# Kernel tuning notes

Measured on AMD Instinct MI355X. Metric: run time of the kernel, lower is better.

The kernel has to match this reference:

```python
import jax, jax.numpy as jnp
import numpy as np

RADIUS = 0.1
K = 32
NUM_GROUPS = 8
EPS = 1e-5
B, N = 2, 4096
IN_DIM = 13
OUT_DIMS = (64, 64, 128)


def _safe_norm(x, axis=-1, keepdims=False):
    # 2-norm with zero (not NaN) gradient at 0; forward identical to jnp.linalg.norm
    sq = jnp.sum(x * x, axis=axis, keepdims=keepdims)
    nz = sq > 0
    return jnp.where(nz, jnp.sqrt(jnp.where(nz, sq, 1.0)), 0.0)


def _angle(v1, v2):
    y = _safe_norm(jnp.cross(v1, v2), axis=-1)
    x = jnp.sum(v1 * v2, axis=-1)
    deg = (y == 0) & (x == 0)  # degenerate pairs (e.g. self-neighbor): atan2(0,0)=0
    return jnp.where(deg, 0.0, jnp.arctan2(y, jnp.where(deg, 1.0, x)))


def _ball_group(xyz, radius, k):
    # xyz: (B,N,3) -> neighbor indices (B,N,K); pad out-of-radius slots with first valid idx
    b, n, _ = xyz.shape
    sq = jnp.sum((xyz[:, :, None, :] - xyz[:, None, :, :]) ** 2, axis=-1)  # (B,N,N)
    idx = jnp.broadcast_to(jnp.arange(n, dtype=jnp.int32), (b, n, n))
    idx = jnp.where(sq > radius * radius, n, idx)
    idx = jnp.sort(idx, axis=-1)[:, :, :k]  # (B,N,K)
    first = idx[:, :, :1]
    return jnp.where(idx == n, first, idx)


def _group_norm(x, gamma, beta):
    # x: (B,C,K,N), torch GroupNorm(8, C) semantics (biased var, eps=1e-5)
    b, c, k, n = x.shape
    xg = x.reshape(b, NUM_GROUPS, c // NUM_GROUPS, k, n)
    m = jnp.mean(xg, axis=(2, 3, 4), keepdims=True)
    v = jnp.var(xg, axis=(2, 3, 4), keepdims=True)
    xn = ((xg - m) * jax.lax.rsqrt(v + EPS)).reshape(b, c, k, n)
    return xn * gamma[None, :, None, None] + beta[None, :, None, None]


def _forward(feature, xyz, conv0_w, gn0_g, gn0_b, conv1_w, gn1_g, gn1_b,
             conv2_w, gn2_g, gn2_b, wa, wb, wc):
    b = xyz.shape[0]
    idx = _ball_group(xyz, RADIUS, K)                     # (B,N,K) int32
    bidx = jnp.arange(b)[:, None, None]
    grouped_xyz = xyz[bidx, idx]                          # (B,N,K,3)
    grouped_xyz1 = grouped_xyz - xyz[:, :, None, :]       # relative coords
    dists = _safe_norm(grouped_xyz1, axis=-1, keepdims=True)
    grouped_n = feature[bidx, idx]                        # grouped normals (B,N,K,3)
    new_points = jnp.concatenate([grouped_xyz1, dists, grouped_n], axis=-1)  # (B,N,K,7)

    nr = feature[:, :, None, :]                           # (B,N,1,3)
    ppf = jnp.stack([_angle(nr, grouped_xyz1),
                     _angle(grouped_n, grouped_xyz1),
                     _angle(nr, grouped_n)], axis=-1)     # (B,N,K,3)

    xyz6 = jnp.concatenate([jnp.broadcast_to(xyz[:, :, None, :], grouped_xyz.shape),
                            grouped_xyz], axis=-1)        # (B,N,K,6)
    fused = jnp.concatenate([wa * xyz6, wb * new_points[..., :4], wc * ppf], axis=-1)  # (B,N,K,13)

    x = jnp.transpose(fused, (0, 3, 2, 1))                # (B,13,K,N)
    layers = [(conv0_w, gn0_g, gn0_b), (conv1_w, gn1_g, gn1_b), (conv2_w, gn2_g, gn2_b)]
    for i, (w, g, bb) in enumerate(layers):
        x = jnp.einsum('oc,bckn->bokn', w, x)             # 1x1 conv, no bias
        x = _group_norm(x, g, bb)
        if i != len(layers) - 1:
            x = jax.nn.relu(x)
    out = jnp.max(jax.nn.relu(x), axis=2)                 # (B,128,N)
    x = jnp.max(x, axis=2)                                # (B,128,N)
    return (out, x)


def setup_inputs() -> dict:
    key = jax.random.key(0)
    ks = jax.random.split(key, 8)
    xyz = jax.random.uniform(ks[0], (B, N, 3), dtype=jnp.float32)
    feature = jax.random.normal(ks[1], (B, N, 3), dtype=jnp.float32)
    feature = feature / _safe_norm(feature, axis=-1, keepdims=True)  # unit normals
    inp = {'feature': feature, 'xyz': xyz}
    dims = [IN_DIM] + list(OUT_DIMS)
    for i in range(3):
        scale = 1.0 / np.sqrt(dims[i])
        inp[f'conv{i}_w'] = (jax.random.normal(ks[2 + i], (dims[i + 1], dims[i]), dtype=jnp.float32) * scale)
        inp[f'gn{i}_g'] = jnp.ones((dims[i + 1],), jnp.float32)
        inp[f'gn{i}_b'] = jnp.zeros((dims[i + 1],), jnp.float32)
    inp['wa'] = jnp.ones((1,), jnp.float32)
    inp['wb'] = jnp.ones((1,), jnp.float32)
    inp['wc'] = jnp.ones((1,), jnp.float32)
    return inp


def reference(feature, xyz, conv0_w, gn0_g, gn0_b, conv1_w, gn1_g, gn1_b,
              conv2_w, gn2_g, gn2_b, wa, wb, wc):
    return _forward(feature, xyz, conv0_w, gn0_g, gn0_b, conv1_w, gn1_g, gn1_b,
                    conv2_w, gn2_g, gn2_b, wa, wb, wc)
```

## Files before the change

kernel.cpp:

```cpp
#include <hip/hip_runtime.h>
#include <hip/hip_bf16.h>

#define DEVINL __device__ __forceinline__

typedef short short8 __attribute__((ext_vector_type(8)));
typedef float f32x4 __attribute__((ext_vector_type(4)));

namespace {
constexpr int NB = 2;
constexpr int NN = 4096;
constexpr int KK = 32;
constexpr int NP = NN * KK;
constexpr float R2 = 0.01f;
constexpr float GEPS = 1e-5f;
}

DEVINL ushort2 splitbf(float v) {
    unsigned int b = __float_as_uint(v);
    unsigned int hb = b & 0xffff0000u;
    float r = v - __uint_as_float(hb);
    unsigned int lb = __float_as_uint(r);
    ushort2 res;
    res.x = (unsigned short)(hb >> 16);
    res.y = (unsigned short)(lb >> 16);
    return res;
}

DEVINL float angle3(float ax, float ay, float az, float bx, float by, float bz) {
    float crx = ay * bz - az * by;
    float cry = az * bx - ax * bz;
    float crz = ax * by - ay * bx;
    float sq = crx * crx + cry * cry + crz * crz;
    float yv = sq > 0.f ? sqrtf(sq) : 0.f;
    float xv = ax * bx + ay * by + az * bz;
    if (yv == 0.f && xv == 0.f) return 0.f;
    return atan2f(yv, xv);
}

template <int NV>
DEVINL float blockReducePart(float* vals) {
    #pragma unroll
    for (int m = 1; m < 64; m <<= 1) {
        #pragma unroll
        for (int q = 0; q < NV; ++q) vals[q] += __shfl_xor(vals[q], m, 64);
    }
    __shared__ float red[4][NV];
    int lane = threadIdx.x & 63, w = threadIdx.x >> 6;
    if (lane == 0) {
        #pragma unroll
        for (int q = 0; q < NV; ++q) red[w][q] = vals[q];
    }
    __syncthreads();
    float v = 0.f;
    if ((int)threadIdx.x < NV)
        v = red[0][threadIdx.x] + red[1][threadIdx.x] +
            red[2][threadIdx.x] + red[3][threadIdx.x];
    return v;
}

__global__ __launch_bounds__(256) void k_red(const float* __restrict__ part,
                                             float* __restrict__ stats, int nblk) {
    int o = blockIdx.x;
    const float* p = part + (size_t)o * nblk;
    float s = 0.f;
    for (int i = threadIdx.x; i < nblk; i += 256) s += p[i];
    #pragma unroll
    for (int m = 1; m < 64; m <<= 1) s += __shfl_xor(s, m, 64);
    __shared__ float r[4];
    if ((threadIdx.x & 63) == 0) r[threadIdx.x >> 6] = s;
    __syncthreads();
    if (threadIdx.x == 0) stats[o] = r[0] + r[1] + r[2] + r[3];
}

__global__ void k_prep(const float* __restrict__ w0, const float* __restrict__ w1,
                       const float* __restrict__ w2, float* __restrict__ w0t,
                       short* __restrict__ a1hi, short* __restrict__ a1lo,
                       short* __restrict__ a2hi, short* __restrict__ a2lo) {
    int t = threadIdx.x;
    for (int x = t; x < 64 * 13; x += 256) { int o = x / 13, c = x % 13; w0t[c * 64 + o] = w0[x]; }
    for (int x = t; x < 512; x += 256) {
        int lane = x & 63, ks = (x >> 6) & 1, mt = x >> 7;
        int o = mt * 16 + (lane & 15);
        int cb = ks * 32 + (lane >> 4) * 8;
        #pragma unroll
        for (int e = 0; e < 8; ++e) {
            ushort2 s = splitbf(w1[o * 64 + cb + e]);
            a1hi[x * 8 + e] = (short)s.x;
            a1lo[x * 8 + e] = (short)s.y;
        }
    }
    for (int x = t; x < 1024; x += 256) {
        int lane = x & 63, ks = (x >> 6) & 1, mt = x >> 7;
        int o = mt * 16 + (lane & 15);
        int cb = ks * 32 + (lane >> 4) * 8;
        #pragma unroll
        for (int e = 0; e < 8; ++e) {
            ushort2 s = splitbf(w2[o * 64 + cb + e]);
            a2hi[x * 8 + e] = (short)s.x;
            a2lo[x * 8 + e] = (short)s.y;
        }
    }
}

__global__ __launch_bounds__(256) void k_ball(const float* __restrict__ xyz,
                                              int* __restrict__ idx) {
    int wid = blockIdx.x * 4 + (threadIdx.x >> 6);
    int lane = threadIdx.x & 63;
    int b = wid >> 12;
    int i = wid & (NN - 1);
    const float* xb = xyz + b * NN * 3;
    float cx = xb[i * 3 + 0], cy = xb[i * 3 + 1], cz = xb[i * 3 + 2];
    int* out = idx + wid * KK;
    int cnt = 0;
    int firstj = 0;
    for (int base = 0; base < NN; base += 64) {
        int j = base + lane;
        float dx = xb[j * 3 + 0] - cx;
        float dy = xb[j * 3 + 1] - cy;
        float dz = xb[j * 3 + 2] - cz;
        float d2 = __fadd_rn(__fadd_rn(__fmul_rn(dx, dx), __fmul_rn(dy, dy)), __fmul_rn(dz, dz));
        bool valid = d2 <= R2;
        unsigned long long m = __ballot(valid);
        if (cnt == 0 && m != 0ull) firstj = base + (int)__builtin_ctzll(m);
        int pos = (int)__popcll(m & ((1ull << lane) - 1ull));
        if (valid && (cnt + pos) < KK) out[cnt + pos] = j;
        cnt += (int)__popcll(m);
        if (cnt >= KK) break;
    }
    if (cnt < KK) {
        int kpad = cnt + lane;
        if (kpad < KK) out[kpad] = firstj;
    }
}

__global__ __launch_bounds__(256) void k_feat(
    const float* __restrict__ xyz, const float* __restrict__ feat,
    const int* __restrict__ idx, const float* __restrict__ w0t,
    const float* __restrict__ wap, const float* __restrict__ wbp,
    const float* __restrict__ wcp, float* __restrict__ f13,
    float* __restrict__ part0) {
    int t = blockIdx.x * 256 + threadIdx.x;
    int b = t / NP, r = t % NP;
    int i = r >> 5;
    int j = idx[t];
    const float* xb = xyz + b * NN * 3;
    const float* fb = feat + b * NN * 3;
    float cx = xb[i * 3], cy = xb[i * 3 + 1], cz = xb[i * 3 + 2];
    float nx = fb[i * 3], ny = fb[i * 3 + 1], nz = fb[i * 3 + 2];
    float gx = xb[j * 3], gy = xb[j * 3 + 1], gz = xb[j * 3 + 2];
    float mx = fb[j * 3], my = fb[j * 3 + 1], mz = fb[j * 3 + 2];
    float dx = gx - cx, dy = gy - cy, dz = gz - cz;
    float d2 = dx * dx + dy * dy + dz * dz;
    float dist = d2 > 0.f ? sqrtf(d2) : 0.f;
    float a1 = angle3(nx, ny, nz, dx, dy, dz);
    float a2 = angle3(mx, my, mz, dx, dy, dz);
    float a3 = angle3(nx, ny, nz, mx, my, mz);
    float WA = wap[0], WB = wbp[0], WC = wcp[0];
    float f[13] = {WA * cx, WA * cy, WA * cz, WA * gx, WA * gy, WA * gz,
                   WB * dx, WB * dy, WB * dz, WB * dist, WC * a1, WC * a2, WC * a3};
    float* fo = f13 + (size_t)b * 13 * NP + r;
    #pragma unroll
    for (int c = 0; c < 13; ++c) fo[(size_t)c * NP] = f[c];
    float acc[64];
    #pragma unroll
    for (int o = 0; o < 64; ++o) acc[o] = 0.f;
    #pragma unroll
    for (int c = 0; c < 13; ++c) {
        float v = f[c];
        const float* wr = w0t + c * 64;
        #pragma unroll
        for (int o = 0; o < 64; ++o) acc[o] = fmaf(wr[o], v, acc[o]);
    }
    float vals[16];
    #pragma unroll
    for (int g = 0; g < 8; ++g) {
        float sv = 0.f, sq = 0.f;
        #pragma unroll
        for (int c2 = 0; c2 < 8; ++c2) { float v = acc[g * 8 + c2]; sv += v; sq = fmaf(v, v, sq); }
        vals[g * 2] = sv; vals[g * 2 + 1] = sq;
    }
    float pv = blockReducePart<16>(vals);
    if ((int)threadIdx.x < 16) {
        int blkInB = blockIdx.x & 511;
        part0[(size_t)(b * 16 + threadIdx.x) * 512 + blkInB] = pv;
    }
}

__global__ __launch_bounds__(256) void k_stats01(
    const float* __restrict__ f13, const float* __restrict__ stats0,
    const float* __restrict__ g0, const float* __restrict__ b0,
    const float* __restrict__ w0t,
    const short* __restrict__ a1hi, const short* __restrict__ a1lo,
    float* __restrict__ part1) {
    __shared__ __align__(16) short Xhi[128 * 64];
    __shared__ __align__(16) short Xlo[128 * 64];
    __shared__ float Aff[128];
    int t = threadIdx.x, blk = blockIdx.x;
    int b = blk >> 10;
    int blkInB = blk & 1023;
    int pbase = blkInB << 7;
    if (t < 64) {
        int c = t, g = c >> 3;
        const float inv = 1.f / 1048576.f;
        float s = stats0[b * 16 + g * 2], q = stats0[b * 16 + g * 2 + 1];
        float mean = s * inv;
        float var = q * inv - mean * mean;
        float rstd = rsqrtf(var + GEPS);
        float a = rstd * g0[c];
        Aff[c] = a; Aff[64 + c] = fmaf(-mean, a, b0[c]);
    }
    __syncthreads();
    {
        int p = t & 127, chalf = t >> 7;
        const float* fi = f13 + (size_t)b * 13 * NP + pbase + p;
        float fv[13];
        #pragma unroll
        for (int c = 0; c < 13; ++c) fv[c] = fi[(size_t)c * NP];
        float acc[32];
        #pragma unroll
        for (int o = 0; o < 32; ++o) acc[o] = 0.f;
        #pragma unroll
        for (int c = 0; c < 13; ++c) {
            const float* wr = w0t + c * 64 + chalf * 32;
            #pragma unroll
            for (int o = 0; o < 32; ++o) acc[o] = fmaf(wr[o], fv[c], acc[o]);
        }
        int swz = (p & 7) << 4;
        #pragma unroll
        for (int jc = 0; jc < 4; ++jc) {
            int hw[4], lw[4];
            #pragma unroll
            for (int u = 0; u < 4; ++u) {
                int o0 = jc * 8 + u * 2;
                int ch0 = chalf * 32 + o0;
                float v0 = fmaxf(fmaf(Aff[ch0], acc[o0], Aff[64 + ch0]), 0.f);
                float v1 = fmaxf(fmaf(Aff[ch0 + 1], acc[o0 + 1], Aff[64 + ch0 + 1]), 0.f);
                ushort2 s0 = splitbf(v0), s1 = splitbf(v1);
                hw[u] = (int)((unsigned)s0.x | ((unsigned)s1.x << 16));
                lw[u] = (int)((unsigned)s0.y | ((unsigned)s1.y << 16));
            }
            int off = p * 128 + ((chalf * 64 + jc * 16) ^ swz);
            *reinterpret_cast<int4*>((char*)Xhi + off) = make_int4(hw[0], hw[1], hw[2], hw[3]);
            *reinterpret_cast<int4*>((char*)Xlo + off) = make_int4(lw[0], lw[1], lw[2], lw[3]);
        }
    }
    __syncthreads();
    {
        int w = t >> 6, lane = t & 63, col = lane & 15, kb = lane >> 4;
        short8 whi[2], wlo[2];
        #pragma unroll
        for (int ks = 0; ks < 2; ++ks) {
            int fi_ = ((w * 2 + ks) * 64 + lane) * 8;
            whi[ks] = *reinterpret_cast<const short8*>(a1hi + fi_);
            wlo[ks] = *reinterpret_cast<const short8*>(a1lo + fi_);
        }
        float sv = 0.f, sq = 0.f;
        int swzr = (col & 7) << 4;
        #pragma unroll 2
        for (int s = 0; s < 8; ++s) {
            int rowoff = (s * 16 + col) * 128;
            f32x4 d = {0.f, 0.f, 0.f, 0.f};
            #pragma unroll
            for (int ks = 0; ks < 2; ++ks) {
                int boff = rowoff + ((ks * 64 + kb * 16) ^ swzr);
                short8 bh = *reinterpret_cast<const short8*>((char*)Xhi + boff);
                short8 bl = *reinterpret_cast<const short8*>((char*)Xlo + boff);
                d = __builtin_amdgcn_mfma_f32_16x16x32_bf16(whi[ks], bh, d, 0, 0, 0);
                d = __builtin_amdgcn_mfma_f32_16x16x32_bf16(whi[ks], bl, d, 0, 0, 0);
                d = __builtin_amdgcn_mfma_f32_16x16x32_bf16(wlo[ks], bh, d, 0, 0, 0);
            }
            #pragma unroll
            for (int q = 0; q < 4; ++q) {
                sv += d[q];
                sq = fmaf(d[q], d[q], sq);
            }
        }
        #pragma unroll
        for (int m = 1; m <= 16; m <<= 1) {
            sv += __shfl_xor(sv, m, 64);
            sq += __shfl_xor(sq, m, 64);
        }
        if ((lane & 31) == 0) {
            int grp = w * 2 + (lane >> 5);
            size_t o = (size_t)(b * 16 + grp * 2) * 1024 + blkInB;
            part1[o] = sv;
            part1[o + 1024] = sq;
        }
    }
}

__global__ __launch_bounds__(256) void k_fused2(
    const float* __restrict__ f13, const float* __restrict__ stats0,
    const float* __restrict__ g0, const float* __restrict__ b0,
    const float* __restrict__ w0t,
    const short* __restrict__ a1hi, const short* __restrict__ a1lo,
    const float* __restrict__ stats1,
    const float* __restrict__ g1, const float* __restrict__ b1,
    const float* __restrict__ g2,
    const short* __restrict__ a2hi, const short* __restrict__ a2lo,
    float* __restrict__ ext, float* __restrict__ part2) {
    __shared__ __align__(16) short Xhi[128 * 64];
    __shared__ __align__(16) short Xlo[128 * 64];
    __shared__ float Aff[256];
    int t = threadIdx.x, blk = blockIdx.x;
    int b = blk >> 10;
    int blkInB = blk & 1023;
    int pbase = blkInB << 7;
    if (t < 64) {
        int c = t, g = c >> 3;
        const float inv = 1.f / 1048576.f;
        float s = stats0[b * 16 + g * 2], q = stats0[b * 16 + g * 2 + 1];
        float mean = s * inv;
        float var = q * inv - mean * mean;
        float rstd = rsqrtf(var + GEPS);
        float a = rstd * g0[c];
        Aff[c] = a; Aff[64 + c] = fmaf(-mean, a, b0[c]);
        float s1 = stats1[b * 16 + g * 2], q1 = stats1[b * 16 + g * 2 + 1];
        float mean1 = s1 * inv;
        float var1 = q1 * inv - mean1 * mean1;
        float rstd1 = rsqrtf(var1 + GEPS);
        float a1 = rstd1 * g1[c];
        Aff[128 + c] = a1; Aff[192 + c] = fmaf(-mean1, a1, b1[c]);
    }
    __syncthreads();
    {
        int p = t & 127, chalf = t >> 7;
        const float* fi = f13 + (size_t)b * 13 * NP + pbase + p;
        float fv[13];
        #pragma unroll
        for (int c = 0; c < 13; ++c) fv[c] = fi[(size_t)c * NP];
        float acc[32];
        #pragma unroll
        for (int o = 0; o < 32; ++o) acc[o] = 0.f;
        #pragma unroll
        for (int c = 0; c < 13; ++c) {
            const float* wr = w0t + c * 64 + chalf * 32;
            #pragma unroll
            for (int o = 0; o < 32; ++o) acc[o] = fmaf(wr[o], fv[c], acc[o]);
        }
        int swz = (p & 7) << 4;
        #pragma unroll
        for (int jc = 0; jc < 4; ++jc) {
            int hw[4], lw[4];
            #pragma unroll
            for (int u = 0; u < 4; ++u) {
                int o0 = jc * 8 + u * 2;
                int ch0 = chalf * 32 + o0;
                float v0 = fmaxf(fmaf(Aff[ch0], acc[o0], Aff[64 + ch0]), 0.f);
                float v1 = fmaxf(fmaf(Aff[ch0 + 1], acc[o0 + 1], Aff[64 + ch0 + 1]), 0.f);
                ushort2 s0 = splitbf(v0), s1 = splitbf(v1);
                hw[u] = (int)((unsigned)s0.x | ((unsigned)s1.x << 16));
                lw[u] = (int)((unsigned)s0.y | ((unsigned)s1.y << 16));
            }
            int off = p * 128 + ((chalf * 64 + jc * 16) ^ swz);
            *reinterpret_cast<int4*>((char*)Xhi + off) = make_int4(hw[0], hw[1], hw[2], hw[3]);
            *reinterpret_cast<int4*>((char*)Xlo + off) = make_int4(lw[0], lw[1], lw[2], lw[3]);
        }
    }
    __syncthreads();
    int w = t >> 6, lane = t & 63, col = lane & 15, kb = lane >> 4;
    int swzr = (col & 7) << 4;
    float y[8][4];
    {
        short8 whi[2], wlo[2];
        #pragma unroll
        for (int ks = 0; ks < 2; ++ks) {
            int fi_ = ((w * 2 + ks) * 64 + lane) * 8;
            whi[ks] = *reinterpret_cast<const short8*>(a1hi + fi_);
            wlo[ks] = *reinterpret_cast<const short8*>(a1lo + fi_);
        }
        #pragma unroll 2
        for (int s = 0; s < 8; ++s) {
            int rowoff = (s * 16 + col) * 128;
            f32x4 d = {0.f, 0.f, 0.f, 0.f};
            #pragma unroll
            for (int ks = 0; ks < 2; ++ks) {
                int boff = rowoff + ((ks * 64 + kb * 16) ^ swzr);
                short8 bh = *reinterpret_cast<const short8*>((char*)Xhi + boff);
                short8 bl = *reinterpret_cast<const short8*>((char*)Xlo + boff);
                d = __builtin_amdgcn_mfma_f32_16x16x32_bf16(whi[ks], bh, d, 0, 0, 0);
                d = __builtin_amdgcn_mfma_f32_16x16x32_bf16(whi[ks], bl, d, 0, 0, 0);
                d = __builtin_amdgcn_mfma_f32_16x16x32_bf16(wlo[ks], bh, d, 0, 0, 0);
            }
            #pragma unroll
            for (int q = 0; q < 4; ++q) y[s][q] = d[q];
        }
    }
    __syncthreads();
    {
        float a1v[4], b1v[4];
        #pragma unroll
        for (int q = 0; q < 4; ++q) {
            int c = w * 16 + kb * 4 + q;
            a1v[q] = Aff[128 + c]; b1v[q] = Aff[192 + c];
        }
        #pragma unroll
        for (int s = 0; s < 8; ++s) {
            int hw[2], lw[2];
            #pragma unroll
            for (int u = 0; u < 2; ++u) {
                float v0 = fmaxf(fmaf(a1v[u * 2], y[s][u * 2], b1v[u * 2]), 0.f);
                float v1 = fmaxf(fmaf(a1v[u * 2 + 1], y[s][u * 2 + 1], b1v[u * 2 + 1]), 0.f);
                ushort2 s0 = splitbf(v0), s1 = splitbf(v1);
                hw[u] = (int)((unsigned)s0.x | ((unsigned)s1.x << 16));
                lw[u] = (int)((unsigned)s0.y | ((unsigned)s1.y << 16));
            }
            int p = s * 16 + col;
            int off = p * 128 + ((w * 32 + kb * 8) ^ swzr);
            *reinterpret_cast<int2*>((char*)Xhi + off) = make_int2(hw[0], hw[1]);
            *reinterpret_cast<int2*>((char*)Xlo + off) = make_int2(lw[0], lw[1]);
        }
    }
    __syncthreads();
    {
        int mt0 = w * 2;
        short8 whi[2][2], wlo[2][2];
        #pragma unroll
        for (int m = 0; m < 2; ++m)
            #pragma unroll
            for (int ks = 0; ks < 2; ++ks) {
                int fi_ = (((mt0 + m) * 2 + ks) * 64 + lane) * 8;
                whi[m][ks] = *reinterpret_cast<const short8*>(a2hi + fi_);
                wlo[m][ks] = *reinterpret_cast<const short8*>(a2lo + fi_);
            }
        float gv[2][4];
        #pragma unroll
        for (int m = 0; m < 2; ++m)
            #pragma unroll
            for (int q = 0; q < 4; ++q) gv[m][q] = g2[(mt0 + m) * 16 + kb * 4 + q];
        float sv[2] = {0.f, 0.f}, sq[2] = {0.f, 0.f};
        int ibase = pbase >> 5;
        #pragma unroll
        for (int sp = 0; sp < 4; ++sp) {
            f32x4 dp0[2], dp1[2];
            #pragma unroll
            for (int ss = 0; ss < 2; ++ss) {
                int rowoff = ((sp * 2 + ss) * 16 + col) * 128;
                short8 bh[2], bl[2];
                #pragma unroll
                for (int ks = 0; ks < 2; ++ks) {
                    int boff = rowoff + ((ks * 64 + kb * 16) ^ swzr);
                    bh[ks] = *reinterpret_cast<const short8*>((char*)Xhi + boff);
                    bl[ks] = *reinterpret_cast<const short8*>((char*)Xlo + boff);
                }
                #pragma unroll
                for (int m = 0; m < 2; ++m) {
                    f32x4 d = {0.f, 0.f, 0.f, 0.f};
                    #pragma unroll
                    for (int ks = 0; ks < 2; ++ks) {
                        d = __builtin_amdgcn_mfma_f32_16x16x32_bf16(whi[m][ks], bh[ks], d, 0, 0, 0);
                        d = __builtin_amdgcn_mfma_f32_16x16x32_bf16(whi[m][ks], bl[ks], d, 0, 0, 0);
                        d = __builtin_amdgcn_mfma_f32_16x16x32_bf16(wlo[m][ks], bh[ks], d, 0, 0, 0);
                    }
                    #pragma unroll
                    for (int q = 0; q < 4; ++q) {
                        sv[m] += d[q];
                        sq[m] = fmaf(d[q], d[q], sq[m]);
                    }
                    if (ss == 0) dp0[m] = d; else dp1[m] = d;
                }
            }
            #pragma unroll
            for (int m = 0; m < 2; ++m) {
                float e[4];
                #pragma unroll
                for (int q = 0; q < 4; ++q) {
                    bool mx = gv[m][q] >= 0.f;
                    e[q] = mx ? fmaxf(dp0[m][q], dp1[m][q]) : fminf(dp0[m][q], dp1[m][q]);
                    #pragma unroll
                    for (int sh = 1; sh <= 8; sh <<= 1) {
                        float o = __shfl_xor(e[q], sh, 64);
                        e[q] = mx ? fmaxf(e[q], o) : fminf(e[q], o);
                    }
                }
                if (col == 0) {
                    #pragma unroll
                    for (int q = 0; q < 4; ++q) {
                        int ch = (mt0 + m) * 16 + kb * 4 + q;
                        ext[((size_t)b * 128 + ch) * NN + ibase + sp] = e[q];
                    }
                }
            }
        }
        #pragma unroll
        for (int m = 0; m < 2; ++m) {
            #pragma unroll
            for (int sh = 1; sh <= 32; sh <<= 1) {
                sv[m] += __shfl_xor(sv[m], sh, 64);
                sq[m] += __shfl_xor(sq[m], sh, 64);
            }
        }
        if (lane == 0) {
            #pragma unroll
            for (int m = 0; m < 2; ++m) {
                size_t o = (size_t)(b * 16 + (mt0 + m) * 2) * 1024 + blkInB;
                part2[o] = sv[m];
                part2[o + 1024] = sq[m];
            }
        }
    }
}

__global__ __launch_bounds__(256) void k_final(
    const float* __restrict__ ext, const float* __restrict__ stats2,
    const float* __restrict__ g2, const float* __restrict__ b2,
    float* __restrict__ outp) {
    __shared__ float A[128], Bc[128];
    int t = blockIdx.x * 256 + threadIdx.x;
    int b = t / (128 * NN);
    int rem = t - b * 128 * NN;
    int c = rem >> 12;
    if (threadIdx.x < 128) {
        int cc = threadIdx.x, g = cc >> 4;
        const float inv = 1.f / 2097152.f;
        float s = stats2[b * 16 + g * 2], q = stats2[b * 16 + g * 2 + 1];
        float mean = s * inv;
        float var = q * inv - mean * mean;
        float rstd = rsqrtf(var + GEPS);
        float a = rstd * g2[cc];
        A[cc] = a; Bc[cc] = fmaf(-mean, a, b2[cc]);
    }
    __syncthreads();
    float v = ext[t];
    float val = fmaf(A[c], v, Bc[c]);
    outp[t] = fmaxf(val, 0.f);
    outp[NB * 128 * NN + t] = val;
}

extern "C" void kernel_launch(void* const* d_in, const int* in_sizes, int n_in,
                              void* d_out, int out_size, void* d_ws, size_t ws_size,
                              hipStream_t stream) {
    const float* feat = (const float*)d_in[0];
    const float* xyz  = (const float*)d_in[1];
    const float* w0 = (const float*)d_in[2];
    const float* g0 = (const float*)d_in[3];
    const float* b0 = (const float*)d_in[4];
    const float* w1 = (const float*)d_in[5];
    const float* g1 = (const float*)d_in[6];
    const float* b1 = (const float*)d_in[7];
    const float* w2 = (const float*)d_in[8];
    const float* g2 = (const float*)d_in[9];
    const float* b2 = (const float*)d_in[10];
    const float* wa = (const float*)d_in[11];
    const float* wb = (const float*)d_in[12];
    const float* wc = (const float*)d_in[13];

    char* ws = (char*)d_ws;
    float* stats = (float*)ws;
    float* w0t  = (float*)(ws + 4096);
    short* a1hi = (short*)(ws + 16384);
    short* a1lo = (short*)(ws + 24576);
    short* a2hi = (short*)(ws + 32768);
    short* a2lo = (short*)(ws + 49152);
    int*   idx  = (int*)(ws + 65536);
    float* part0 = (float*)(ws + 1179648);
    float* part1 = (float*)(ws + 1245184);
    float* part2 = (float*)(ws + 1376256);
    float* f13  = (float*)(ws + (2ull << 20));
    float* ext  = (float*)(ws + (16ull << 20));

    hipLaunchKernelGGL(k_prep, dim3(1), dim3(256), 0, stream,
                       w0, w1, w2, w0t, a1hi, a1lo, a2hi, a2lo);
    hipLaunchKernelGGL(k_ball, dim3((NB * NN) / 4), dim3(256), 0, stream, xyz, idx);
    hipLaunchKernelGGL(k_feat, dim3((NB * NP) / 256), dim3(256), 0, stream,
                       xyz, feat, idx, w0t, wa, wb, wc, f13, part0);
    hipLaunchKernelGGL(k_red, dim3(32), dim3(256), 0, stream, part0, stats, 512);
    hipLaunchKernelGGL(k_stats01, dim3((NB * NP) / 128), dim3(256), 0, stream,
                       f13, stats, g0, b0, w0t, a1hi, a1lo, part1);
    hipLaunchKernelGGL(k_red, dim3(32), dim3(256), 0, stream, part1, stats + 32, 1024);
    hipLaunchKernelGGL(k_fused2, dim3((NB * NP) / 128), dim3(256), 0, stream,
                       f13, stats, g0, b0, w0t, a1hi, a1lo,
                       stats + 32, g1, b1, g2, a2hi, a2lo, ext, part2);
    hipLaunchKernelGGL(k_red, dim3(32), dim3(256), 0, stream, part2, stats + 64, 1024);
    hipLaunchKernelGGL(k_final, dim3((NB * 128 * NN) / 256), dim3(256), 0, stream,
                       ext, stats + 64, g2, b2, (float*)d_out);
}
```

Baseline: 217.8 us.

## Fold stat reductions into consumer kernels and merge prep into ball query

Removes the three small k_red launches by having each consumer block redundantly reduce the per-block partial sums for its batch into shared memory. The weight-prep kernel is merged into block 0 of the ball-query kernel, and k_final now processes four elements per thread with a quarter of the blocks. This cuts launch count and inter-kernel gaps, at the cost of every block re-reading 8K–16K partial floats (L2-resident) before starting work.

New measurement: 328.0 us. +50.6%, slower.

```diff
diff --git a/kernel.cpp b/kernel.cpp
--- a/kernel.cpp
+++ b/kernel.cpp
@@ -58,52 +58,52 @@
     return v;
 }
 
-__global__ __launch_bounds__(256) void k_red(const float* __restrict__ part,
-                                             float* __restrict__ stats, int nblk) {
-    int o = blockIdx.x;
-    const float* p = part + (size_t)o * nblk;
-    float s = 0.f;
-    for (int i = threadIdx.x; i < nblk; i += 256) s += p[i];
-    #pragma unroll
-    for (int m = 1; m < 64; m <<= 1) s += __shfl_xor(s, m, 64);
-    __shared__ float r[4];
-    if ((threadIdx.x & 63) == 0) r[threadIdx.x >> 6] = s;
-    __syncthreads();
-    if (threadIdx.x == 0) stats[o] = r[0] + r[1] + r[2] + r[3];
-}
-
-__global__ void k_prep(const float* __restrict__ w0, const float* __restrict__ w1,
-                       const float* __restrict__ w2, float* __restrict__ w0t,
-                       short* __restrict__ a1hi, short* __restrict__ a1lo,
-                       short* __restrict__ a2hi, short* __restrict__ a2lo) {
-    int t = threadIdx.x;
-    for (int x = t; x < 64 * 13; x += 256) { int o = x / 13, c = x % 13; w0t[c * 64 + o] = w0[x]; }
-    for (int x = t; x < 512; x += 256) {
-        int lane = x & 63, ks = (x >> 6) & 1, mt = x >> 7;
-        int o = mt * 16 + (lane & 15);
-        int cb = ks * 32 + (lane >> 4) * 8;
-        #pragma unroll
-        for (int e = 0; e < 8; ++e) {
-            ushort2 s = splitbf(w1[o * 64 + cb + e]);
-            a1hi[x * 8 + e] = (short)s.x;
-            a1lo[x * 8 + e] = (short)s.y;
-        }
-    }
-    for (int x = t; x < 1024; x += 256) {
-        int lane = x & 63, ks = (x >> 6) & 1, mt = x >> 7;
-        int o = mt * 16 + (lane & 15);
-        int cb = ks * 32 + (lane >> 4) * 8;
-        #pragma unroll
-        for (int e = 0; e < 8; ++e) {
-            ushort2 s = splitbf(w2[o * 64 + cb + e]);
-            a2hi[x * 8 + e] = (short)s.x;
-            a2lo[x * 8 + e] = (short)s.y;
-        }
-    }
-}
-
-__global__ __launch_bounds__(256) void k_ball(const float* __restrict__ xyz,
-                                              int* __restrict__ idx) {
+template <int NSLOT>
+DEVINL void selfReduce(const float* __restrict__ part, int b, float* statsL) {
+    int w = threadIdx.x >> 6, lane = threadIdx.x & 63;
+    #pragma unroll
+    for (int o = w; o < 16; o += 4) {
+        const float* p = part + (size_t)(b * 16 + o) * NSLOT;
+        float s = 0.f;
+        for (int i = lane; i < NSLOT; i += 64) s += p[i];
+        #pragma unroll
+        for (int m = 1; m < 64; m <<= 1) s += __shfl_xor(s, m, 64);
+        if (lane == 0) statsL[o] = s;
+    }
+}
+
+__global__ __launch_bounds__(256) void k_ballprep(
+    const float* __restrict__ xyz, int* __restrict__ idx,
+    const float* __restrict__ w0, const float* __restrict__ w1,
+    const float* __restrict__ w2, float* __restrict__ w0t,
+    short* __restrict__ a1hi, short* __restrict__ a1lo,
+    short* __restrict__ a2hi, short* __restrict__ a2lo) {
+    if (blockIdx.x == 0) {
+        int t = threadIdx.x;
+        for (int x = t; x < 64 * 13; x += 256) { int o = x / 13, c = x % 13; w0t[c * 64 + o] = w0[x]; }
+        for (int x = t; x < 512; x += 256) {
+            int lane = x & 63, ks = (x >> 6) & 1, mt = x >> 7;
+            int o = mt * 16 + (lane & 15);
+            int cb = ks * 32 + (lane >> 4) * 8;
+            #pragma unroll
+            for (int e = 0; e < 8; ++e) {
+                ushort2 s = splitbf(w1[o * 64 + cb + e]);
+                a1hi[x * 8 + e] = (short)s.x;
+                a1lo[x * 8 + e] = (short)s.y;
+            }
+        }
+        for (int x = t; x < 1024; x += 256) {
+            int lane = x & 63, ks = (x >> 6) & 1, mt = x >> 7;
+            int o = mt * 16 + (lane & 15);
+            int cb = ks * 32 + (lane >> 4) * 8;
+            #pragma unroll
+            for (int e = 0; e < 8; ++e) {
+                ushort2 s = splitbf(w2[o * 64 + cb + e]);
+                a2hi[x * 8 + e] = (short)s.x;
+                a2lo[x * 8 + e] = (short)s.y;
+            }
+        }
+    }
     int wid = blockIdx.x * 4 + (threadIdx.x >> 6);
     int lane = threadIdx.x & 63;
     int b = wid >> 12;
@@ -187,7 +187,7 @@
 }
 
 __global__ __launch_bounds__(256) void k_stats01(
-    const float* __restrict__ f13, const float* __restrict__ stats0,
+    const float* __restrict__ f13, const float* __restrict__ part0,
     const float* __restrict__ g0, const float* __restrict__ b0,
     const float* __restrict__ w0t,
     const short* __restrict__ a1hi, const short* __restrict__ a1lo,
@@ -195,16 +195,18 @@
     __shared__ __align__(16) short Xhi[128 * 64];
     __shared__ __align__(16) short Xlo[128 * 64];
     __shared__ float Aff[128];
+    __shared__ float statsL[16];
     int t = threadIdx.x, blk = blockIdx.x;
     int b = blk >> 10;
     int blkInB = blk & 1023;
     int pbase = blkInB << 7;
+    selfReduce<512>(part0, b, statsL);
+    __syncthreads();
     if (t < 64) {
         int c = t, g = c >> 3;
         const float inv = 1.f / 1048576.f;
-        float s = stats0[b * 16 + g * 2], q = stats0[b * 16 + g * 2 + 1];
-        float mean = s * inv;
-        float var = q * inv - mean * mean;
+        float mean = statsL[g * 2] * inv;
+        float var = statsL[g * 2 + 1] * inv - mean * mean;
         float rstd = rsqrtf(var + GEPS);
         float a = rstd * g0[c];
         Aff[c] = a; Aff[64 + c] = fmaf(-mean, a, b0[c]);
@@ -290,11 +292,11 @@
 }
 
 __global__ __launch_bounds__(256) void k_fused2(
-    const float* __restrict__ f13, const float* __restrict__ stats0,
+    const float* __restrict__ f13, const float* __restrict__ part0,
+    const float* __restrict__ part1,
     const float* __restrict__ g0, const float* __restrict__ b0,
     const float* __restrict__ w0t,
     const short* __restrict__ a1hi, const short* __restrict__ a1lo,
-    const float* __restrict__ stats1,
     const float* __restrict__ g1, const float* __restrict__ b1,
     const float* __restrict__ g2,
     const short* __restrict__ a2hi, const short* __restrict__ a2lo,
@@ -302,25 +304,33 @@
     __shared__ __align__(16) short Xhi[128 * 64];
     __shared__ __align__(16) short Xlo[128 * 64];
     __shared__ float Aff[256];
+    __shared__ float statsL[16];
     int t = threadIdx.x, blk = blockIdx.x;
     int b = blk >> 10;
     int blkInB = blk & 1023;
     int pbase = blkInB << 7;
+    selfReduce<512>(part0, b, statsL);
+    __syncthreads();
     if (t < 64) {
         int c = t, g = c >> 3;
         const float inv = 1.f / 1048576.f;
-        float s = stats0[b * 16 + g * 2], q = stats0[b * 16 + g * 2 + 1];
-        float mean = s * inv;
-        float var = q * inv - mean * mean;
+        float mean = statsL[g * 2] * inv;
+        float var = statsL[g * 2 + 1] * inv - mean * mean;
         float rstd = rsqrtf(var + GEPS);
         float a = rstd * g0[c];
         Aff[c] = a; Aff[64 + c] = fmaf(-mean, a, b0[c]);
-        float s1 = stats1[b * 16 + g * 2], q1 = stats1[b * 16 + g * 2 + 1];
-        float mean1 = s1 * inv;
-        float var1 = q1 * inv - mean1 * mean1;
-        float rstd1 = rsqrtf(var1 + GEPS);
-        float a1 = rstd1 * g1[c];
-        Aff[128 + c] = a1; Aff[192 + c] = fmaf(-mean1, a1, b1[c]);
+    }
+    __syncthreads();
+    selfReduce<1024>(part1, b, statsL);
+    __syncthreads();
+    if (t < 64) {
+        int c = t, g = c >> 3;
+        const float inv = 1.f / 1048576.f;
+        float mean = statsL[g * 2] * inv;
+        float var = statsL[g * 2 + 1] * inv - mean * mean;
+        float rstd = rsqrtf(var + GEPS);
+        float a1 = rstd * g1[c];
+        Aff[128 + c] = a1; Aff[192 + c] = fmaf(-mean, a1, b1[c]);
     }
     __syncthreads();
     {
@@ -502,36 +512,43 @@
 }
 
 __global__ __launch_bounds__(256) void k_final(
-    const float* __restrict__ ext, const float* __restrict__ stats2,
+    const float* __restrict__ ext, const float* __restrict__ part2,
     const float* __restrict__ g2, const float* __restrict__ b2,
     float* __restrict__ outp) {
+    __shared__ float statsL[16];
     __shared__ float A[128], Bc[128];
-    int t = blockIdx.x * 256 + threadIdx.x;
-    int b = t / (128 * NN);
-    int rem = t - b * 128 * NN;
-    int c = rem >> 12;
-    if (threadIdx.x < 128) {
-        int cc = threadIdx.x, g = cc >> 4;
+    int tid = threadIdx.x, blk = blockIdx.x;
+    int b = blk >> 9;
+    selfReduce<1024>(part2, b, statsL);
+    __syncthreads();
+    if (tid < 128) {
+        int g = tid >> 4;
         const float inv = 1.f / 2097152.f;
-        float s = stats2[b * 16 + g * 2], q = stats2[b * 16 + g * 2 + 1];
-        float mean = s * inv;
-        float var = q * inv - mean * mean;
+        float mean = statsL[g * 2] * inv;
+        float var = statsL[g * 2 + 1] * inv - mean * mean;
         float rstd = rsqrtf(var + GEPS);
-        float a = rstd * g2[cc];
-        A[cc] = a; Bc[cc] = fmaf(-mean, a, b2[cc]);
-    }
-    __syncthreads();
-    float v = ext[t];
-    float val = fmaf(A[c], v, Bc[c]);
-    outp[t] = fmaxf(val, 0.f);
-    outp[NB * 128 * NN + t] = val;
+        float a = rstd * g2[tid];
+        A[tid] = a; Bc[tid] = fmaf(-mean, a, b2[tid]);
+    }
+    __syncthreads();
+    const size_t TOT = (size_t)NB * 128 * NN;
+    #pragma unroll
+    for (int e = 0; e < 4; ++e) {
+        int t = blk * 1024 + e * 256 + tid;
+        int rem = t - b * (128 * NN);
+        int c = rem >> 12;
+        float v = ext[t];
+        float val = fmaf(A[c], v, Bc[c]);
+        outp[t] = fmaxf(val, 0.f);
+        outp[TOT + t] = val;
+    }
 }
 
 extern "C" void kernel_launch(void* const* d_in, const int* in_sizes, int n_in,
                               void* d_out, int out_size, void* d_ws, size_t ws_size,
                               hipStream_t stream) {
-    const float* feat = (const float*)d_in[0];
-    const float* xyz  = (const float*)d_in[1];
+    const float* featp = (const float*)d_in[0];
+    const float* xyzp  = (const float*)d_in[1];
     const float* w0 = (const float*)d_in[2];
     const float* g0 = (const float*)d_in[3];
     const float* b0 = (const float*)d_in[4];
@@ -541,12 +558,11 @@
     const float* w2 = (const float*)d_in[8];
     const float* g2 = (const float*)d_in[9];
     const float* b2 = (const float*)d_in[10];
-    const float* wa = (const float*)d_in[11];
-    const float* wb = (const float*)d_in[12];
-    const float* wc = (const float*)d_in[13];
+    const float* wap = (const float*)d_in[11];
+    const float* wbp = (const float*)d_in[12];
+    const float* wcp = (const float*)d_in[13];
 
     char* ws = (char*)d_ws;
-    float* stats = (float*)ws;
     float* w0t  = (float*)(ws + 4096);
     short* a1hi = (short*)(ws + 16384);
     short* a1lo = (short*)(ws + 24576);
@@ -559,19 +575,15 @@
     float* f13  = (float*)(ws + (2ull << 20));
     float* ext  = (float*)(ws + (16ull << 20));
 
-    hipLaunchKernelGGL(k_prep, dim3(1), dim3(256), 0, stream,
-                       w0, w1, w2, w0t, a1hi, a1lo, a2hi, a2lo);
-    hipLaunchKernelGGL(k_ball, dim3((NB * NN) / 4), dim3(256), 0, stream, xyz, idx);
+    hipLaunchKernelGGL(k_ballprep, dim3((NB * NN) / 4), dim3(256), 0, stream,
+                       xyzp, idx, w0, w1, w2, w0t, a1hi, a1lo, a2hi, a2lo);
     hipLaunchKernelGGL(k_feat, dim3((NB * NP) / 256), dim3(256), 0, stream,
-                       xyz, feat, idx, w0t, wa, wb, wc, f13, part0);
-    hipLaunchKernelGGL(k_red, dim3(32), dim3(256), 0, stream, part0, stats, 512);
+                       xyzp, featp, idx, w0t, wap, wbp, wcp, f13, part0);
     hipLaunchKernelGGL(k_stats01, dim3((NB * NP) / 128), dim3(256), 0, stream,
-                       f13, stats, g0, b0, w0t, a1hi, a1lo, part1);
-    hipLaunchKernelGGL(k_red, dim3(32), dim3(256), 0, stream, part1, stats + 32, 1024);
+                       f13, part0, g0, b0, w0t, a1hi, a1lo, part1);
     hipLaunchKernelGGL(k_fused2, dim3((NB * NP) / 128), dim3(256), 0, stream,
-                       f13, stats, g0, b0, w0t, a1hi, a1lo,
-                       stats + 32, g1, b1, g2, a2hi, a2lo, ext, part2);
-    hipLaunchKernelGGL(k_red, dim3(32), dim3(256), 0, stream, part2, stats + 64, 1024);
-    hipLaunchKernelGGL(k_final, dim3((NB * 128 * NN) / 256), dim3(256), 0, stream,
-                       ext, stats + 64, g2, b2, (float*)d_out);
-}
+                       f13, part0, part1, g0, b0, w0t, a1hi, a1lo,
+                       g1, b1, g2, a2hi, a2lo, ext, part2);
+    hipLaunchKernelGGL(k_final, dim3((NB * 128 * NN) / 1024), dim3(256), 0, stream,
+                       ext, part2, g2, b2, (float*)d_out);
+}
```

## Fuse weight prep and ball query into feature kernel via shared-memory indices

Applied to the files above, without the earlier changes.

Merges the weight-prep, ball-query and feature kernels into one launch. Each block runs the ball query for its 8 centre points, keeps the neighbour indices in shared memory instead of a global buffer, and stages w0 transposed in LDS for the first conv. The f13 loads in the two later kernels are moved ahead of the stats/affine setup so they overlap with it. This removes two launches and the idx round trip through global memory. In exchange, block 0 carries the serial weight-prep work, and per-block ball-query latency now sits in front of the feature compute.

Result: slower. 229.5 us (+5.4%).

```diff
diff --git a/kernel.cpp b/kernel.cpp
--- a/kernel.cpp
+++ b/kernel.cpp
@@ -72,78 +72,78 @@
     if (threadIdx.x == 0) stats[o] = r[0] + r[1] + r[2] + r[3];
 }
 
-__global__ void k_prep(const float* __restrict__ w0, const float* __restrict__ w1,
-                       const float* __restrict__ w2, float* __restrict__ w0t,
-                       short* __restrict__ a1hi, short* __restrict__ a1lo,
-                       short* __restrict__ a2hi, short* __restrict__ a2lo) {
-    int t = threadIdx.x;
-    for (int x = t; x < 64 * 13; x += 256) { int o = x / 13, c = x % 13; w0t[c * 64 + o] = w0[x]; }
-    for (int x = t; x < 512; x += 256) {
-        int lane = x & 63, ks = (x >> 6) & 1, mt = x >> 7;
-        int o = mt * 16 + (lane & 15);
-        int cb = ks * 32 + (lane >> 4) * 8;
-        #pragma unroll
-        for (int e = 0; e < 8; ++e) {
-            ushort2 s = splitbf(w1[o * 64 + cb + e]);
-            a1hi[x * 8 + e] = (short)s.x;
-            a1lo[x * 8 + e] = (short)s.y;
-        }
-    }
-    for (int x = t; x < 1024; x += 256) {
-        int lane = x & 63, ks = (x >> 6) & 1, mt = x >> 7;
-        int o = mt * 16 + (lane & 15);
-        int cb = ks * 32 + (lane >> 4) * 8;
-        #pragma unroll
-        for (int e = 0; e < 8; ++e) {
-            ushort2 s = splitbf(w2[o * 64 + cb + e]);
-            a2hi[x * 8 + e] = (short)s.x;
-            a2lo[x * 8 + e] = (short)s.y;
-        }
-    }
-}
-
-__global__ __launch_bounds__(256) void k_ball(const float* __restrict__ xyz,
-                                              int* __restrict__ idx) {
-    int wid = blockIdx.x * 4 + (threadIdx.x >> 6);
-    int lane = threadIdx.x & 63;
-    int b = wid >> 12;
-    int i = wid & (NN - 1);
+__global__ __launch_bounds__(256) void k_feat2(
+    const float* __restrict__ xyz, const float* __restrict__ feat,
+    const float* __restrict__ w0, const float* __restrict__ w1,
+    const float* __restrict__ w2,
+    const float* __restrict__ wap, const float* __restrict__ wbp,
+    const float* __restrict__ wcp,
+    float* __restrict__ w0t, short* __restrict__ a1hi, short* __restrict__ a1lo,
+    short* __restrict__ a2hi, short* __restrict__ a2lo,
+    float* __restrict__ f13, float* __restrict__ part0) {
+    __shared__ int idxL[8][32];
+    __shared__ float wL[13 * 64];
+    int tid = threadIdx.x, blk = blockIdx.x;
+    int b = blk >> 9;
+    int blkInB = blk & 511;
+    if (blk == 0) {
+        for (int x = tid; x < 64 * 13; x += 256) { int o = x / 13, c = x % 13; w0t[c * 64 + o] = w0[x]; }
+        for (int x = tid; x < 512; x += 256) {
+            int lane = x & 63, ks = (x >> 6) & 1, mt = x >> 7;
+            int o = mt * 16 + (lane & 15);
+            int cb = ks * 32 + (lane >> 4) * 8;
+            #pragma unroll
+            for (int e = 0; e < 8; ++e) {
+                ushort2 s = splitbf(w1[o * 64 + cb + e]);
+                a1hi[x * 8 + e] = (short)s.x;
+                a1lo[x * 8 + e] = (short)s.y;
+            }
+        }
+        for (int x = tid; x < 1024; x += 256) {
+            int lane = x & 63, ks = (x >> 6) & 1, mt = x >> 7;
+            int o = mt * 16 + (lane & 15);
+            int cb = ks * 32 + (lane >> 4) * 8;
+            #pragma unroll
+            for (int e = 0; e < 8; ++e) {
+                ushort2 s = splitbf(w2[o * 64 + cb + e]);
+                a2hi[x * 8 + e] = (short)s.x;
+                a2lo[x * 8 + e] = (short)s.y;
+            }
+        }
+    }
+    for (int x = tid; x < 832; x += 256) { int o = x / 13, c = x % 13; wL[c * 64 + o] = w0[x]; }
+    int wv = tid >> 6, lane = tid & 63;
     const float* xb = xyz + b * NN * 3;
-    float cx = xb[i * 3 + 0], cy = xb[i * 3 + 1], cz = xb[i * 3 + 2];
-    int* out = idx + wid * KK;
-    int cnt = 0;
-    int firstj = 0;
-    for (int base = 0; base < NN; base += 64) {
-        int j = base + lane;
-        float dx = xb[j * 3 + 0] - cx;
-        float dy = xb[j * 3 + 1] - cy;
-        float dz = xb[j * 3 + 2] - cz;
-        float d2 = __fadd_rn(__fadd_rn(__fmul_rn(dx, dx), __fmul_rn(dy, dy)), __fmul_rn(dz, dz));
-        bool valid = d2 <= R2;
-        unsigned long long m = __ballot(valid);
-        if (cnt == 0 && m != 0ull) firstj = base + (int)__builtin_ctzll(m);
-        int pos = (int)__popcll(m & ((1ull << lane) - 1ull));
-        if (valid && (cnt + pos) < KK) out[cnt + pos] = j;
-        cnt += (int)__popcll(m);
-        if (cnt >= KK) break;
-    }
-    if (cnt < KK) {
-        int kpad = cnt + lane;
-        if (kpad < KK) out[kpad] = firstj;
-    }
-}
-
-__global__ __launch_bounds__(256) void k_feat(
-    const float* __restrict__ xyz, const float* __restrict__ feat,
-    const int* __restrict__ idx, const float* __restrict__ w0t,
-    const float* __restrict__ wap, const float* __restrict__ wbp,
-    const float* __restrict__ wcp, float* __restrict__ f13,
-    float* __restrict__ part0) {
-    int t = blockIdx.x * 256 + threadIdx.x;
-    int b = t / NP, r = t % NP;
+    #pragma unroll
+    for (int pp = 0; pp < 2; ++pp) {
+        int pt = wv * 2 + pp;
+        int i = blkInB * 8 + pt;
+        float cx = xb[i * 3 + 0], cy = xb[i * 3 + 1], cz = xb[i * 3 + 2];
+        int cnt = 0;
+        int firstj = 0;
+        for (int base = 0; base < NN; base += 64) {
+            int j = base + lane;
+            float dx = xb[j * 3 + 0] - cx;
+            float dy = xb[j * 3 + 1] - cy;
+            float dz = xb[j * 3 + 2] - cz;
+            float d2 = __fadd_rn(__fadd_rn(__fmul_rn(dx, dx), __fmul_rn(dy, dy)), __fmul_rn(dz, dz));
+            bool valid = d2 <= R2;
+            unsigned long long m = __ballot(valid);
+            if (cnt == 0 && m != 0ull) firstj = base + (int)__builtin_ctzll(m);
+            int pos = (int)__popcll(m & ((1ull << lane) - 1ull));
+            if (valid && (cnt + pos) < KK) idxL[pt][cnt + pos] = j;
+            cnt += (int)__popcll(m);
+            if (cnt >= KK) break;
+        }
+        if (cnt < KK) {
+            int kpad = cnt + lane;
+            if (kpad < KK) idxL[pt][kpad] = firstj;
+        }
+    }
+    __syncthreads();
+    int r = blkInB * 256 + tid;
     int i = r >> 5;
-    int j = idx[t];
-    const float* xb = xyz + b * NN * 3;
+    int j = idxL[tid >> 5][tid & 31];
     const float* fb = feat + b * NN * 3;
     float cx = xb[i * 3], cy = xb[i * 3 + 1], cz = xb[i * 3 + 2];
     float nx = fb[i * 3], ny = fb[i * 3 + 1], nz = fb[i * 3 + 2];
@@ -167,7 +167,7 @@
     #pragma unroll
     for (int c = 0; c < 13; ++c) {
         float v = f[c];
-        const float* wr = w0t + c * 64;
+        const float* wr = wL + c * 64;
         #pragma unroll
         for (int o = 0; o < 64; ++o) acc[o] = fmaf(wr[o], v, acc[o]);
     }
@@ -180,10 +180,7 @@
         vals[g * 2] = sv; vals[g * 2 + 1] = sq;
     }
     float pv = blockReducePart<16>(vals);
-    if ((int)threadIdx.x < 16) {
-        int blkInB = blockIdx.x & 511;
-        part0[(size_t)(b * 16 + threadIdx.x) * 512 + blkInB] = pv;
-    }
+    if (tid < 16) part0[(size_t)(b * 16 + tid) * 512 + blkInB] = pv;
 }
 
 __global__ __launch_bounds__(256) void k_stats01(
@@ -199,6 +196,11 @@
     int b = blk >> 10;
     int blkInB = blk & 1023;
     int pbase = blkInB << 7;
+    int p = t & 127, chalf = t >> 7;
+    const float* fi = f13 + (size_t)b * 13 * NP + pbase + p;
+    float fv[13];
+    #pragma unroll
+    for (int c = 0; c < 13; ++c) fv[c] = fi[(size_t)c * NP];
     if (t < 64) {
         int c = t, g = c >> 3;
         const float inv = 1.f / 1048576.f;
@@ -211,11 +213,6 @@
     }
     __syncthreads();
     {
-        int p = t & 127, chalf = t >> 7;
-        const float* fi = f13 + (size_t)b * 13 * NP + pbase + p;
-        float fv[13];
-        #pragma unroll
-        for (int c = 0; c < 13; ++c) fv[c] = fi[(size_t)c * NP];
         float acc[32];
         #pragma unroll
         for (int o = 0; o < 32; ++o) acc[o] = 0.f;
@@ -306,6 +303,11 @@
     int b = blk >> 10;
     int blkInB = blk & 1023;
     int pbase = blkInB << 7;
+    int p = t & 127, chalf = t >> 7;
+    const float* fi = f13 + (size_t)b * 13 * NP + pbase + p;
+    float fv[13];
+    #pragma unroll
+    for (int c = 0; c < 13; ++c) fv[c] = fi[(size_t)c * NP];
     if (t < 64) {
         int c = t, g = c >> 3;
         const float inv = 1.f / 1048576.f;
@@ -324,11 +326,6 @@
     }
     __syncthreads();
     {
-        int p = t & 127, chalf = t >> 7;
-        const float* fi = f13 + (size_t)b * 13 * NP + pbase + p;
-        float fv[13];
-        #pragma unroll
-        for (int c = 0; c < 13; ++c) fv[c] = fi[(size_t)c * NP];
         float acc[32];
         #pragma unroll
         for (int o = 0; o < 32; ++o) acc[o] = 0.f;
@@ -405,8 +402,8 @@
                 hw[u] = (int)((unsigned)s0.x | ((unsigned)s1.x << 16));
                 lw[u] = (int)((unsigned)s0.y | ((unsigned)s1.y << 16));
             }
-            int p = s * 16 + col;
-            int off = p * 128 + ((w * 32 + kb * 8) ^ swzr);
+            int pp = s * 16 + col;
+            int off = pp * 128 + ((w * 32 + kb * 8) ^ swzr);
             *reinterpret_cast<int2*>((char*)Xhi + off) = make_int2(hw[0], hw[1]);
             *reinterpret_cast<int2*>((char*)Xlo + off) = make_int2(lw[0], lw[1]);
         }
@@ -530,8 +527,8 @@
 extern "C" void kernel_launch(void* const* d_in, const int* in_sizes, int n_in,
                               void* d_out, int out_size, void* d_ws, size_t ws_size,
                               hipStream_t stream) {
-    const float* feat = (const float*)d_in[0];
-    const float* xyz  = (const float*)d_in[1];
+    const float* featp = (const float*)d_in[0];
+    const float* xyzp  = (const float*)d_in[1];
     const float* w0 = (const float*)d_in[2];
     const float* g0 = (const float*)d_in[3];
     const float* b0 = (const float*)d_in[4];
@@ -541,9 +538,9 @@
     const float* w2 = (const float*)d_in[8];
     const float* g2 = (const float*)d_in[9];
     const float* b2 = (const float*)d_in[10];
-    const float* wa = (const float*)d_in[11];
-    const float* wb = (const float*)d_in[12];
-    const float* wc = (const float*)d_in[13];
+    const float* wap = (const float*)d_in[11];
+    const float* wbp = (const float*)d_in[12];
+    const float* wcp = (const float*)d_in[13];
 
     char* ws = (char*)d_ws;
     float* stats = (float*)ws;
@@ -552,18 +549,15 @@
     short* a1lo = (short*)(ws + 24576);
     short* a2hi = (short*)(ws + 32768);
     short* a2lo = (short*)(ws + 49152);
-    int*   idx  = (int*)(ws + 65536);
     float* part0 = (float*)(ws + 1179648);
     float* part1 = (float*)(ws + 1245184);
     float* part2 = (float*)(ws + 1376256);
     float* f13  = (float*)(ws + (2ull << 20));
     float* ext  = (float*)(ws + (16ull << 20));
 
-    hipLaunchKernelGGL(k_prep, dim3(1), dim3(256), 0, stream,
-                       w0, w1, w2, w0t, a1hi, a1lo, a2hi, a2lo);
-    hipLaunchKernelGGL(k_ball, dim3((NB * NN) / 4), dim3(256), 0, stream, xyz, idx);
-    hipLaunchKernelGGL(k_feat, dim3((NB * NP) / 256), dim3(256), 0, stream,
-                       xyz, feat, idx, w0t, wa, wb, wc, f13, part0);
+    hipLaunchKernelGGL(k_feat2, dim3((NB * NP) / 256), dim3(256), 0, stream,
+                       xyzp, featp, w0, w1, w2, wap, wbp, wcp,
+                       w0t, a1hi, a1lo, a2hi, a2lo, f13, part0);
     hipLaunchKernelGGL(k_red, dim3(32), dim3(256), 0, stream, part0, stats, 512);
     hipLaunchKernelGGL(k_stats01, dim3((NB * NP) / 128), dim3(256), 0, stream,
                        f13, stats, g0, b0, w0t, a1hi, a1lo, part1);
```
